# Kernel tuning notes

Measured on AMD Instinct MI355X. Metric: run time of the kernel, lower is better.

## Reference

```python
import jax, jax.numpy as jnp
import numpy as np

B, N, D, H, W = 2, 6, 120, 32, 88
C = 128
Z, HO, WO = 1, 128, 128  # bev_feat_shape
N_POINTS = 1_000_000


def setup_inputs() -> dict:
    key = jax.random.key(0)
    k1, k2, k3, k4, k5 = jax.random.split(key, 5)
    depth = jax.random.normal(k1, (B, N, D, H, W), dtype=jnp.float32)
    feat = jax.random.normal(k2, (B, N, C, H, W), dtype=jnp.float32)
    ranks_depth = jax.random.randint(k3, (N_POINTS,), 0, B * N * D * H * W, dtype=jnp.int32)
    ranks_feat = jax.random.randint(k4, (N_POINTS,), 0, B * N * H * W, dtype=jnp.int32)
    ranks_bev = jnp.sort(jax.random.randint(k5, (N_POINTS,), 0, B * Z * HO * WO, dtype=jnp.int32))
    # Derive intervals (consecutive runs of equal ranks_bev), as the CUDA op expects.
    rb = np.asarray(ranks_bev)
    starts = np.concatenate([[0], np.nonzero(np.diff(rb))[0] + 1]).astype(np.int32)
    lengths = np.diff(np.concatenate([starts, [rb.shape[0]]])).astype(np.int32)
    return {
        "depth": depth,
        "feat": feat,
        "ranks_depth": ranks_depth,
        "ranks_feat": ranks_feat,
        "ranks_bev": ranks_bev,
        "interval_starts": jnp.asarray(starts),
        "interval_lengths": jnp.asarray(lengths),
    }


def reference(depth, feat, ranks_depth, ranks_feat, ranks_bev, interval_starts, interval_lengths):
    b, n, c, h, w = feat.shape
    # feat laid out [b,n,c,h,w]; ranks_feat indexes (b,n,h,w) positions -> put c last.
    feat_flat = feat.transpose(0, 1, 3, 4, 2).reshape(-1, c)  # [b*n*h*w, c]
    depth_flat = depth.reshape(-1)                            # [b*n*d*h*w]
    # Gather depth scalar and feature row per point, multiply.
    prod = depth_flat[ranks_depth][:, None] * feat_flat[ranks_feat]  # [n_points, c]
    # Interval-based accumulation == segment-sum over sorted ranks_bev.
    num_cells = b * Z * HO * WO
    out = jax.ops.segment_sum(prod, ranks_bev, num_segments=num_cells)  # [b*z*h*w, c]
    out = out.reshape(b, Z, HO, WO, c).transpose(0, 4, 1, 2, 3)  # [b, c, z, h, w]
    return out
```

## Files before the change

kernel.cpp:

```cpp
#include <hip/hip_runtime.h>
#include <hip/hip_bf16.h>

#define HW_    2816
#define C_     128
#define BN_    12
#define SPAT_  16384
#define CELLS_ 32768

__device__ __forceinline__ unsigned int f2bf_rne(float x) {
    const unsigned int u = __float_as_uint(x);
    return (u + 0x7fffu + ((u >> 16) & 1u)) >> 16;
}

__global__ __launch_bounds__(256) void transpose_feat_bf16_k(const float* __restrict__ feat,
                                                             __hip_bfloat16* __restrict__ featT) {
    __shared__ float tile[32][33];
    const int bn  = blockIdx.z;
    const int hw0 = blockIdx.x * 32;
    const int c0  = blockIdx.y * 32;
    const int x = threadIdx.x;
    const int y = threadIdx.y;

    const float* src = feat + ((size_t)bn * C_ + c0) * HW_ + hw0;
    #pragma unroll
    for (int yy = y; yy < 32; yy += 8)
        tile[yy][x] = src[(size_t)yy * HW_ + x];
    __syncthreads();
    __hip_bfloat16* dst = featT + ((size_t)bn * HW_ + hw0) * C_ + c0;
    #pragma unroll
    for (int yy = y; yy < 32; yy += 8)
        dst[(size_t)yy * C_ + x] = __float2bfloat16(tile[x][yy]);
}

__global__ __launch_bounds__(256) void depth_pregather_k(const float* __restrict__ depth,
                                                         const int* __restrict__ rd,
                                                         float* __restrict__ dper, int n) {
    const int tid    = blockIdx.x * 256 + threadIdx.x;
    const int stride = gridDim.x * 256;
    for (int base = tid; base < n; base += 4 * stride) {
        int ii[4], idx[4];
        float v[4];
        #pragma unroll
        for (int u = 0; u < 4; ++u) {
            ii[u] = base + u * stride;
            idx[u] = rd[ii[u] < n ? ii[u] : base];
        }
        #pragma unroll
        for (int u = 0; u < 4; ++u) v[u] = depth[idx[u]];
        #pragma unroll
        for (int u = 0; u < 4; ++u) if (ii[u] < n) dper[ii[u]] = v[u];
    }
}

__global__ __launch_bounds__(256) void bevpool_half_k(const float* __restrict__ dper,
                                                      const uint4* __restrict__ featT,
                                                      const int* __restrict__ rf_arr,
                                                      const int* __restrict__ rb,
                                                      const int* __restrict__ istart,
                                                      const int* __restrict__ ilen,
                                                      unsigned short* __restrict__ cellbuf,
                                                      int n_intervals) {
    const int half = blockIdx.x & 1;
    const int widx = threadIdx.x >> 6;
    const int ivl  = (blockIdx.x >> 1) * 4 + widx;
    if (ivl >= n_intervals) return;
    const int lane = threadIdx.x & 63;
    const int grp  = lane >> 3;
    const int sl   = lane & 7;

    const int start = istart[ivl];
    const int end   = start + ilen[ivl];
    const int cell  = rb[start];

    float acc[8] = {0.f, 0.f, 0.f, 0.f, 0.f, 0.f, 0.f, 0.f};
    const size_t hoff = (size_t)(half * 8 + sl);

    for (int i = start + grp; i < end; i += 32) {
        int cl_[4], rf_[4];
        float d_[4];
        uint4 f_[4];
        #pragma unroll
        for (int u = 0; u < 4; ++u) {
            const int ii = i + 8 * u;
            cl_[u] = (ii < end) ? ii : i;
        }
        #pragma unroll
        for (int u = 0; u < 4; ++u) rf_[u] = rf_arr[cl_[u]];
        #pragma unroll
        for (int u = 0; u < 4; ++u) d_[u] = dper[cl_[u]];
        #pragma unroll
        for (int u = 1; u < 4; ++u) d_[u] = (i + 8 * u < end) ? d_[u] : 0.f;
        #pragma unroll
        for (int u = 0; u < 4; ++u) f_[u] = featT[(size_t)rf_[u] * 16 + hoff];
        #pragma unroll
        for (int u = 0; u < 4; ++u) {
            const float d = d_[u];
            acc[0] = fmaf(d, __uint_as_float(f_[u].x << 16),         acc[0]);
            acc[1] = fmaf(d, __uint_as_float(f_[u].x & 0xffff0000u), acc[1]);
            acc[2] = fmaf(d, __uint_as_float(f_[u].y << 16),         acc[2]);
            acc[3] = fmaf(d, __uint_as_float(f_[u].y & 0xffff0000u), acc[3]);
            acc[4] = fmaf(d, __uint_as_float(f_[u].z << 16),         acc[4]);
            acc[5] = fmaf(d, __uint_as_float(f_[u].z & 0xffff0000u), acc[5]);
            acc[6] = fmaf(d, __uint_as_float(f_[u].w << 16),         acc[6]);
            acc[7] = fmaf(d, __uint_as_float(f_[u].w & 0xffff0000u), acc[7]);
        }
    }

    #pragma unroll
    for (int c = 0; c < 8; ++c) {
        acc[c] += __shfl_down(acc[c], 32);
        acc[c] += __shfl_down(acc[c], 16);
        acc[c] += __shfl_down(acc[c], 8);
    }

    if (grp == 0) {
        uint4 p;
        p.x = f2bf_rne(acc[0]) | (f2bf_rne(acc[1]) << 16);
        p.y = f2bf_rne(acc[2]) | (f2bf_rne(acc[3]) << 16);
        p.z = f2bf_rne(acc[4]) | (f2bf_rne(acc[5]) << 16);
        p.w = f2bf_rne(acc[6]) | (f2bf_rne(acc[7]) << 16);
        *(uint4*)(cellbuf + (size_t)cell * C_ + half * 64 + sl * 8) = p;
    }
}

__global__ __launch_bounds__(256) void transpose_out_bf16_k(const unsigned short* __restrict__ cellbuf,
                                                            float* __restrict__ out) {
    __shared__ float tile[32][33];
    const int b   = blockIdx.z;
    const int sp0 = blockIdx.x * 32;
    const int c0  = blockIdx.y * 32;
    const int x = threadIdx.x;
    const int y = threadIdx.y;

    const unsigned short* src = cellbuf + ((size_t)b * SPAT_ + sp0) * C_ + c0;
    #pragma unroll
    for (int yy = y; yy < 32; yy += 8)
        tile[yy][x] = __uint_as_float((unsigned int)src[(size_t)yy * C_ + x] << 16);
    __syncthreads();
    float* dst = out + ((size_t)b * C_ + c0) * SPAT_ + sp0;
    #pragma unroll
    for (int yy = y; yy < 32; yy += 8)
        dst[(size_t)yy * SPAT_ + x] = tile[x][yy];
}

__global__ __launch_bounds__(256) void bevpool_fallback_k(const float* __restrict__ depth,
                                                          const float* __restrict__ feat,
                                                          const int* __restrict__ rd_arr,
                                                          const int* __restrict__ rf_arr,
                                                          const int* __restrict__ rb,
                                                          const int* __restrict__ istart,
                                                          const int* __restrict__ ilen,
                                                          float* __restrict__ out,
                                                          int n_intervals) {
    const int wave = (int)((blockIdx.x * blockDim.x + threadIdx.x) >> 6);
    const int lane = threadIdx.x & 63;
    if (wave >= n_intervals) return;
    const int start = istart[wave];
    const int len   = ilen[wave];
    const int cell  = rb[start];
    float ax = 0.f, ay = 0.f;
    const int end = start + len;
    for (int i = start; i < end; ++i) {
        const int rfi = rf_arr[i];
        const int bn  = rfi / HW_;
        const int hw  = rfi - bn * HW_;
        const float d = depth[rd_arr[i]];
        const float* frow = feat + (size_t)bn * (C_ * HW_) + hw;
        ax = fmaf(d, frow[(size_t)(2 * lane)     * HW_], ax);
        ay = fmaf(d, frow[(size_t)(2 * lane + 1) * HW_], ay);
    }
    const int b  = cell >> 14;
    const int sp = cell & (SPAT_ - 1);
    float* o = out + (size_t)b * ((size_t)C_ * SPAT_) + sp;
    o[(size_t)(2 * lane)     * SPAT_] = ax;
    o[(size_t)(2 * lane + 1) * SPAT_] = ay;
}

extern "C" void kernel_launch(void* const* d_in, const int* in_sizes, int n_in,
                              void* d_out, int out_size, void* d_ws, size_t ws_size,
                              hipStream_t stream) {
    const float* depth  = (const float*)d_in[0];
    const float* feat   = (const float*)d_in[1];
    const int*   rd     = (const int*)d_in[2];
    const int*   rf     = (const int*)d_in[3];
    const int*   rb     = (const int*)d_in[4];
    const int*   istart = (const int*)d_in[5];
    const int*   ilen   = (const int*)d_in[6];
    float*       out    = (float*)d_out;
    const int n_intervals = in_sizes[5];
    const int n_points    = in_sizes[2];

    const size_t cellbuf_bytes = (size_t)CELLS_ * C_ * sizeof(unsigned short);
    const size_t featT_bytes   = (size_t)BN_ * HW_ * C_ * sizeof(__hip_bfloat16);
    const size_t dper_bytes    = (size_t)n_points * sizeof(float);

    if (ws_size >= cellbuf_bytes + featT_bytes + dper_bytes) {
        unsigned short* cellbuf = (unsigned short*)d_ws;
        __hip_bfloat16* featT   = (__hip_bfloat16*)((char*)d_ws + cellbuf_bytes);
        float*          dper    = (float*)((char*)d_ws + cellbuf_bytes + featT_bytes);

        hipMemsetAsync(cellbuf, 0, cellbuf_bytes, stream);
        {
            dim3 g(HW_ / 32, C_ / 32, BN_);
            dim3 b(32, 8);
            transpose_feat_bf16_k<<<g, b, 0, stream>>>(feat, featT);
        }
        depth_pregather_k<<<1024, 256, 0, stream>>>(depth, rd, dper, n_points);

        const int blocks2 = 2 * ((n_intervals + 3) / 4);
        bevpool_half_k<<<blocks2, 256, 0, stream>>>(
            dper, (const uint4*)featT, rf, rb, istart, ilen, cellbuf, n_intervals);
        {
            dim3 g(SPAT_ / 32, C_ / 32, 2);
            dim3 b(32, 8);
            transpose_out_bf16_k<<<g, b, 0, stream>>>(cellbuf, out);
        }
    } else {
        hipMemsetAsync(out, 0, (size_t)out_size * sizeof(float), stream);
        const int blocks = (n_intervals + 3) / 4;
        bevpool_fallback_k<<<blocks, 256, 0, stream>>>(
            depth, feat, rd, rf, rb, istart, ilen, out, n_intervals);
    }
}
```

Before: 72.55 us.

## Fuse prep stages into one kernel and pack depth+feat index per point

Merges the feature transpose, depth pregather, interval metadata packing and cellbuf zeroing into a single heterogeneous prep kernel, removing a memset and separate launches. Each point's depth is now stored as bf16 in the high half of a 32-bit word whose low half holds ranks_feat, so the pooling kernel does one 4-byte load per point instead of two. Interval start, length and cell are packed into an int4 for one load per warp. This lowers depth precision to bf16 and assumes ranks_feat fits in 16 bits (max 33792, which fits).

```diff
diff --git a/kernel.cpp b/kernel.cpp
--- a/kernel.cpp
+++ b/kernel.cpp
@@ -7,59 +7,83 @@
 #define SPAT_  16384
 #define CELLS_ 32768
 
+#define TF_BX     88
+#define TF_BY     4
+#define TF_BLOCKS (TF_BX * TF_BY * BN_)
+#define PG_BLOCKS 1024
+#define IV_BLOCKS 128
+#define ZB_BLOCKS 512
+
 __device__ __forceinline__ unsigned int f2bf_rne(float x) {
     const unsigned int u = __float_as_uint(x);
     return (u + 0x7fffu + ((u >> 16) & 1u)) >> 16;
 }
 
-__global__ __launch_bounds__(256) void transpose_feat_bf16_k(const float* __restrict__ feat,
-                                                             __hip_bfloat16* __restrict__ featT) {
+__global__ __launch_bounds__(256) void prep_k(
+        const float* __restrict__ feat, __hip_bfloat16* __restrict__ featT,
+        const float* __restrict__ depth, const int* __restrict__ rd,
+        const int* __restrict__ rf, unsigned int* __restrict__ pair, int n_points,
+        const int* __restrict__ istart, const int* __restrict__ ilen,
+        const int* __restrict__ rb, int4* __restrict__ iv4, int n_intervals,
+        uint4* __restrict__ zbuf, int zb_n16) {
     __shared__ float tile[32][33];
-    const int bn  = blockIdx.z;
-    const int hw0 = blockIdx.x * 32;
-    const int c0  = blockIdx.y * 32;
-    const int x = threadIdx.x;
-    const int y = threadIdx.y;
-
-    const float* src = feat + ((size_t)bn * C_ + c0) * HW_ + hw0;
-    #pragma unroll
-    for (int yy = y; yy < 32; yy += 8)
-        tile[yy][x] = src[(size_t)yy * HW_ + x];
-    __syncthreads();
-    __hip_bfloat16* dst = featT + ((size_t)bn * HW_ + hw0) * C_ + c0;
-    #pragma unroll
-    for (int yy = y; yy < 32; yy += 8)
-        dst[(size_t)yy * C_ + x] = __float2bfloat16(tile[x][yy]);
-}
-
-__global__ __launch_bounds__(256) void depth_pregather_k(const float* __restrict__ depth,
-                                                         const int* __restrict__ rd,
-                                                         float* __restrict__ dper, int n) {
-    const int tid    = blockIdx.x * 256 + threadIdx.x;
-    const int stride = gridDim.x * 256;
-    for (int base = tid; base < n; base += 4 * stride) {
-        int ii[4], idx[4];
-        float v[4];
-        #pragma unroll
-        for (int u = 0; u < 4; ++u) {
-            ii[u] = base + u * stride;
-            idx[u] = rd[ii[u] < n ? ii[u] : base];
-        }
-        #pragma unroll
-        for (int u = 0; u < 4; ++u) v[u] = depth[idx[u]];
-        #pragma unroll
-        for (int u = 0; u < 4; ++u) if (ii[u] < n) dper[ii[u]] = v[u];
-    }
-}
-
-__global__ __launch_bounds__(256) void bevpool_half_k(const float* __restrict__ dper,
-                                                      const uint4* __restrict__ featT,
-                                                      const int* __restrict__ rf_arr,
-                                                      const int* __restrict__ rb,
-                                                      const int* __restrict__ istart,
-                                                      const int* __restrict__ ilen,
-                                                      unsigned short* __restrict__ cellbuf,
-                                                      int n_intervals) {
+    const int bid = blockIdx.x;
+    const int tid = threadIdx.x;
+
+    if (bid < TF_BLOCKS) {
+        const int bn  = bid / (TF_BX * TF_BY);
+        const int r   = bid - bn * (TF_BX * TF_BY);
+        const int c0  = (r / TF_BX) * 32;
+        const int hw0 = (r - (r / TF_BX) * TF_BX) * 32;
+        const int x = tid & 31, y = tid >> 5;
+        const float* src = feat + ((size_t)bn * C_ + c0) * HW_ + hw0;
+        #pragma unroll
+        for (int yy = y; yy < 32; yy += 8)
+            tile[yy][x] = src[(size_t)yy * HW_ + x];
+        __syncthreads();
+        __hip_bfloat16* dst = featT + ((size_t)bn * HW_ + hw0) * C_ + c0;
+        #pragma unroll
+        for (int yy = y; yy < 32; yy += 8)
+            dst[(size_t)yy * C_ + x] = __float2bfloat16(tile[x][yy]);
+    } else if (bid < TF_BLOCKS + PG_BLOCKS) {
+        const int t = (bid - TF_BLOCKS) * 256 + tid;
+        const int stride = PG_BLOCKS * 256;
+        for (int base = t; base < n_points; base += 4 * stride) {
+            int ii[4], idx[4], rfv[4];
+            float v[4];
+            #pragma unroll
+            for (int u = 0; u < 4; ++u) {
+                ii[u] = base + u * stride;
+                const int cl = ii[u] < n_points ? ii[u] : base;
+                idx[u] = rd[cl];
+                rfv[u] = rf[cl];
+            }
+            #pragma unroll
+            for (int u = 0; u < 4; ++u) v[u] = depth[idx[u]];
+            #pragma unroll
+            for (int u = 0; u < 4; ++u)
+                if (ii[u] < n_points)
+                    pair[ii[u]] = (f2bf_rne(v[u]) << 16) | (unsigned)rfv[u];
+        }
+    } else if (bid < TF_BLOCKS + PG_BLOCKS + IV_BLOCKS) {
+        const int ivl = (bid - TF_BLOCKS - PG_BLOCKS) * 256 + tid;
+        if (ivl < n_intervals) {
+            const int s = istart[ivl];
+            iv4[ivl] = make_int4(s, ilen[ivl], rb[s], 0);
+        }
+    } else {
+        int i = (bid - TF_BLOCKS - PG_BLOCKS - IV_BLOCKS) * 256 + tid;
+        for (; i < zb_n16; i += ZB_BLOCKS * 256)
+            zbuf[i] = make_uint4(0u, 0u, 0u, 0u);
+    }
+}
+
+__global__ __launch_bounds__(256) void bevpool_half_k(
+        const unsigned int* __restrict__ pair,
+        const uint4* __restrict__ featT,
+        const int4* __restrict__ iv4,
+        unsigned short* __restrict__ cellbuf,
+        int n_intervals) {
     const int half = blockIdx.x & 1;
     const int widx = threadIdx.x >> 6;
     const int ivl  = (blockIdx.x >> 1) * 4 + widx;
@@ -68,15 +92,17 @@
     const int grp  = lane >> 3;
     const int sl   = lane & 7;
 
-    const int start = istart[ivl];
-    const int end   = start + ilen[ivl];
-    const int cell  = rb[start];
+    const int4 v    = iv4[ivl];
+    const int start = v.x;
+    const int end   = v.x + v.y;
+    const int cell  = v.z;
 
     float acc[8] = {0.f, 0.f, 0.f, 0.f, 0.f, 0.f, 0.f, 0.f};
     const size_t hoff = (size_t)(half * 8 + sl);
 
     for (int i = start + grp; i < end; i += 32) {
-        int cl_[4], rf_[4];
+        int cl_[4];
+        unsigned pr_[4];
         float d_[4];
         uint4 f_[4];
         #pragma unroll
@@ -85,13 +111,14 @@
             cl_[u] = (ii < end) ? ii : i;
         }
         #pragma unroll
-        for (int u = 0; u < 4; ++u) rf_[u] = rf_arr[cl_[u]];
-        #pragma unroll
-        for (int u = 0; u < 4; ++u) d_[u] = dper[cl_[u]];
+        for (int u = 0; u < 4; ++u) pr_[u] = pair[cl_[u]];
+        #pragma unroll
+        for (int u = 0; u < 4; ++u) d_[u] = __uint_as_float(pr_[u] & 0xffff0000u);
         #pragma unroll
         for (int u = 1; u < 4; ++u) d_[u] = (i + 8 * u < end) ? d_[u] : 0.f;
         #pragma unroll
-        for (int u = 0; u < 4; ++u) f_[u] = featT[(size_t)rf_[u] * 16 + hoff];
+        for (int u = 0; u < 4; ++u)
+            f_[u] = featT[(size_t)(pr_[u] & 0xffffu) * 16 + hoff];
         #pragma unroll
         for (int u = 0; u < 4; ++u) {
             const float d = d_[u];
@@ -192,24 +219,26 @@
 
     const size_t cellbuf_bytes = (size_t)CELLS_ * C_ * sizeof(unsigned short);
     const size_t featT_bytes   = (size_t)BN_ * HW_ * C_ * sizeof(__hip_bfloat16);
-    const size_t dper_bytes    = (size_t)n_points * sizeof(float);
-
-    if (ws_size >= cellbuf_bytes + featT_bytes + dper_bytes) {
+    const size_t pair_bytes    = ((size_t)n_points * sizeof(unsigned int) + 15) & ~(size_t)15;
+    const size_t iv4_bytes     = (size_t)CELLS_ * sizeof(int4);
+
+    if (ws_size >= cellbuf_bytes + featT_bytes + pair_bytes + iv4_bytes &&
+        n_intervals <= CELLS_) {
         unsigned short* cellbuf = (unsigned short*)d_ws;
         __hip_bfloat16* featT   = (__hip_bfloat16*)((char*)d_ws + cellbuf_bytes);
-        float*          dper    = (float*)((char*)d_ws + cellbuf_bytes + featT_bytes);
-
-        hipMemsetAsync(cellbuf, 0, cellbuf_bytes, stream);
-        {
-            dim3 g(HW_ / 32, C_ / 32, BN_);
-            dim3 b(32, 8);
-            transpose_feat_bf16_k<<<g, b, 0, stream>>>(feat, featT);
-        }
-        depth_pregather_k<<<1024, 256, 0, stream>>>(depth, rd, dper, n_points);
+        unsigned int*   pair    = (unsigned int*)((char*)d_ws + cellbuf_bytes + featT_bytes);
+        int4*           iv4     = (int4*)((char*)d_ws + cellbuf_bytes + featT_bytes + pair_bytes);
+
+        const int prep_blocks = TF_BLOCKS + PG_BLOCKS + IV_BLOCKS + ZB_BLOCKS;
+        prep_k<<<prep_blocks, 256, 0, stream>>>(
+            feat, featT, depth, rd, rf, pair, n_points,
+            istart, ilen, rb, iv4, n_intervals,
+            (uint4*)cellbuf, (int)(cellbuf_bytes / 16));
 
         const int blocks2 = 2 * ((n_intervals + 3) / 4);
         bevpool_half_k<<<blocks2, 256, 0, stream>>>(
-            dper, (const uint4*)featT, rf, rb, istart, ilen, cellbuf, n_intervals);
+            pair, (const uint4*)featT, iv4, cellbuf, n_intervals);
+
         {
             dim3 g(SPAT_ / 32, C_ / 32, 2);
             dim3 b(32, 8);
```

New measurement: 63.32 us. 1.15x faster.
